# Optimization experiments

Hardware: AMD Instinct MI355X
Metric: run time of the kernel (lower is better)

The kernel has to match this reference:

```python
import jax, jax.numpy as jnp
import numpy as np

NUM_EXPERTS_TOTAL = 9  # 8 routed + 1 shared (shared expert is also routed via softmax in this module)
TOP_K = 2


def setup_inputs() -> dict:
    key = jax.random.key(0)
    k0, k1, k2, k3, k4 = jax.random.split(key, 5)
    B, S, H, I = 2, 2048, 1024, 2816
    E = NUM_EXPERTS_TOTAL
    x = jax.random.normal(k0, (B, S, H), dtype=jnp.float32)
    Wr = (jax.random.normal(k1, (H, E), dtype=jnp.float32) * 0.02)          # router (no bias)
    Wg = (jax.random.normal(k2, (E, H, I), dtype=jnp.float32) * 0.02)       # gate_proj per expert
    Wu = (jax.random.normal(k3, (E, H, I), dtype=jnp.float32) * 0.02)       # up_proj per expert
    Wd = (jax.random.normal(k4, (E, I, H), dtype=jnp.float32) * 0.02)       # down_proj per expert
    return {"x": x, "Wr": Wr, "Wg": Wg, "Wu": Wu, "Wd": Wd}


def reference(x, Wr, Wg, Wu, Wd):
    B, S, H = x.shape
    E = NUM_EXPERTS_TOTAL
    T = B * S

    # Router: softmax over all 9 experts, then top-2 and renormalize
    logits = jnp.einsum('bsh,he->bse', x, Wr)
    probs = jax.nn.softmax(logits, axis=-1)
    topk_w, topk_idx = jax.lax.top_k(probs, TOP_K)                 # [B,S,K]
    topk_w = topk_w / jnp.sum(topk_w, axis=-1, keepdims=True)

    xf = x.reshape(T, H)
    wf = topk_w.reshape(T, TOP_K)
    idxf = topk_idx.reshape(T, TOP_K)

    # Per-token combine weight for each expert (0 if not selected)
    cw = jnp.zeros((T, E), dtype=x.dtype).at[jnp.arange(T)[:, None], idxf].add(wf)  # [T,E]

    # SwiGLU MLP for every expert (tokens with cw==0 contribute nothing)
    gate = jax.nn.silu(jnp.einsum('th,ehi->tei', xf, Wg))          # [T,E,I]
    hidden = gate * jnp.einsum('th,ehi->tei', xf, Wu)              # [T,E,I]
    out = jnp.einsum('tei,eih,te->th', hidden, Wd, cw)             # weighted combine
    return out.reshape(B, S, H)
```

## Files before the change

### kernel.cpp

```cpp
#include <hip/hip_runtime.h>
#include <cstdint>
#include <cstddef>

#define T_TOK 4096
#define H_DIM 1024
#define I_DIM 2816
#define E_NUM 9
#define MAXTILE 76

typedef __bf16 bf16;
typedef bf16 bf16x4 __attribute__((ext_vector_type(4)));
typedef bf16 bf16x8 __attribute__((ext_vector_type(8)));
typedef float f32x4 __attribute__((ext_vector_type(4)));

constexpr int BM = 128, BN = 128, BK = 32;
constexpr int HTILE = BM * BK;
constexpr size_t HI = (size_t)H_DIM * I_DIM;

constexpr int XCAST_BLKS  = T_TOK * H_DIM / 2048;
constexpr int TGU_BLKS    = (I_DIM / 64) * (H_DIM / 64) * 2 * E_NUM;
constexpr int TD_BLKS     = (H_DIM / 64) * (I_DIM / 64) * E_NUM;
constexpr int ROUTER_BLKS = T_TOK / 4;
constexpr int PRE_BLKS    = XCAST_BLKS + TGU_BLKS + TD_BLKS + ROUTER_BLKS;

#define GL16(gp, lp)                                                                   \
  __builtin_amdgcn_global_load_lds((const __attribute__((address_space(1))) void*)(gp), \
                                   (__attribute__((address_space(3))) void*)(lp), 16, 0, 0)

__device__ __forceinline__ void transpose_tile(const float* __restrict__ src,
                                               bf16* __restrict__ dst, int R, int C,
                                               int bx, int by) {
  __shared__ float tile[64 * 64];
  int r0 = by * 64, c0 = bx * 64;
  int t = threadIdx.x;
#pragma unroll
  for (int h = 0; h < 4; ++h) {
    int idx = h * 256 + t;
    int row = idx >> 4;
    int col = (idx & 15) * 4;
    GL16(src + (size_t)(r0 + row) * C + c0 + col, &tile[idx * 4]);
  }
  __syncthreads();
  int oc = t >> 2;
  int q  = t & 3;
  bf16x8 w0, w1;
#pragma unroll
  for (int j = 0; j < 8; ++j) w0[j] = (bf16)tile[(q * 16 + j) * 64 + oc];
#pragma unroll
  for (int j = 0; j < 8; ++j) w1[j] = (bf16)tile[(q * 16 + 8 + j) * 64 + oc];
  bf16* dp = dst + (size_t)(c0 + oc) * R + r0 + q * 16;
  *reinterpret_cast<bf16x8*>(dp)     = w0;
  *reinterpret_cast<bf16x8*>(dp + 8) = w1;
}

__global__ __launch_bounds__(256) void k_prepass(const float* __restrict__ x,
                                                 bf16* __restrict__ xb,
                                                 const float* __restrict__ Wg,
                                                 const float* __restrict__ Wu,
                                                 const float* __restrict__ Wd,
                                                 bf16* __restrict__ WgT,
                                                 bf16* __restrict__ WuT,
                                                 bf16* __restrict__ WdT,
                                                 const float* __restrict__ Wr,
                                                 int* __restrict__ ridx,
                                                 float* __restrict__ rw,
                                                 int* __restrict__ counts) {
  int b = blockIdx.x;

  if (b < XCAST_BLKS) {
    size_t i = ((size_t)b * 256 + threadIdx.x) * 8;
    float4 a = *reinterpret_cast<const float4*>(x + i);
    float4 c = *reinterpret_cast<const float4*>(x + i + 4);
    bf16x8 v;
    v[0]=(bf16)a.x; v[1]=(bf16)a.y; v[2]=(bf16)a.z; v[3]=(bf16)a.w;
    v[4]=(bf16)c.x; v[5]=(bf16)c.y; v[6]=(bf16)c.z; v[7]=(bf16)c.w;
    *reinterpret_cast<bf16x8*>(xb + i) = v;
    return;
  }
  b -= XCAST_BLKS;

  if (b < TGU_BLKS) {
    int bx = b % (I_DIM / 64);
    int rest = b / (I_DIM / 64);
    int by = rest % (H_DIM / 64);
    int z  = rest / (H_DIM / 64);
    const float* src = (z < 9) ? (Wg + (size_t)z * HI) : (Wu + (size_t)(z - 9) * HI);
    bf16* dst = (z < 9) ? (WgT + (size_t)z * HI) : (WuT + (size_t)(z - 9) * HI);
    transpose_tile(src, dst, H_DIM, I_DIM, bx, by);
    return;
  }
  b -= TGU_BLKS;

  if (b < TD_BLKS) {
    int bx = b % (H_DIM / 64);
    int rest = b / (H_DIM / 64);
    int by = rest % (I_DIM / 64);
    int z  = rest / (I_DIM / 64);
    transpose_tile(Wd + (size_t)z * HI, WdT + (size_t)z * HI, I_DIM, H_DIM, bx, by);
    return;
  }
  b -= TD_BLKS;

  {
    int lane = threadIdx.x & 63;
    int wid  = threadIdx.x >> 6;
    int t = b * 4 + wid;
    const float* xr = x + (size_t)t * H_DIM;
    float acc[E_NUM];
#pragma unroll
    for (int e = 0; e < E_NUM; ++e) acc[e] = 0.f;
    for (int h = lane; h < H_DIM; h += 64) {
      float xv = xr[h];
      const float* wr = Wr + h * E_NUM;
#pragma unroll
      for (int e = 0; e < E_NUM; ++e) acc[e] += xv * wr[e];
    }
#pragma unroll
    for (int off = 32; off > 0; off >>= 1) {
#pragma unroll
      for (int e = 0; e < E_NUM; ++e) acc[e] += __shfl_xor(acc[e], off);
    }
    if (lane == 0) {
      int i0 = 0;
#pragma unroll
      for (int e = 1; e < E_NUM; ++e) if (acc[e] > acc[i0]) i0 = e;
      int i1 = (i0 == 0) ? 1 : 0;
#pragma unroll
      for (int e = 0; e < E_NUM; ++e) if (e != i0 && acc[e] > acc[i1]) i1 = e;
      float r  = expf(acc[i1] - acc[i0]);
      float w0 = 1.f / (1.f + r);
      float w1 = r / (1.f + r);
      ridx[2 * t]     = i0;
      ridx[2 * t + 1] = i1;
      rw[2 * t]     = w0;
      rw[2 * t + 1] = w1;
      atomicAdd(&counts[i0], 1);
      atomicAdd(&counts[i1], 1);
    }
  }
}

__global__ void k_scan(const int* __restrict__ counts, int* __restrict__ offsets,
                       int* __restrict__ cursor, int* __restrict__ tiles,
                       int* __restrict__ n_tiles) {
  if (threadIdx.x == 0) {
    int s = 0, nt = 0;
    for (int e = 0; e < E_NUM; ++e) {
      offsets[e] = s;
      int c = counts[e];
      for (int pt = 0; pt * BM < c && nt < MAXTILE; ++pt) tiles[nt++] = (e << 16) | pt;
      s += c;
    }
    offsets[E_NUM] = s;
    *n_tiles = nt;
  }
  if (threadIdx.x < E_NUM) cursor[threadIdx.x] = 0;
}

__global__ __launch_bounds__(256) void k_scatter(const int* __restrict__ ridx,
                                                 const int* __restrict__ offsets,
                                                 int* __restrict__ cursor,
                                                 int* __restrict__ perm) {
  int t = blockIdx.x * 256 + threadIdx.x;
  if (t >= T_TOK) return;
#pragma unroll
  for (int k = 0; k < 2; ++k) {
    int e = ridx[2 * t + k];
    int pos = atomicAdd(&cursor[e], 1);
    perm[offsets[e] + pos] = 2 * t + k;
  }
}

__global__ __launch_bounds__(256, 2) void k_gateup(const bf16* __restrict__ xb,
                                                   const bf16* __restrict__ WgT,
                                                   const bf16* __restrict__ WuT,
                                                   const int* __restrict__ perm,
                                                   const int* __restrict__ offsets,
                                                   const int* __restrict__ tiles,
                                                   const int* __restrict__ n_tiles,
                                                   bf16* __restrict__ hidden) {
  if ((int)blockIdx.y >= *n_tiles) return;
  int tv = tiles[blockIdx.y];
  int e = tv >> 16, pt = tv & 0xffff;
  int seg0 = offsets[e], cnt = offsets[e + 1] - seg0;
  int n0 = blockIdx.x * BN;

  __shared__ bf16 As[2 * HTILE];
  __shared__ bf16 Bg[2 * HTILE];
  __shared__ bf16 Bu[2 * HTILE];

  int tid = threadIdx.x, lane = tid & 63, wid = tid >> 6;
  int wm = wid >> 1, wn = wid & 1, l15 = lane & 15, l16 = lane >> 4;

  int srow1 = tid >> 2, srow2 = 64 + srow1;
  int kc = (tid & 3) * 8;
  int p1 = pt * BM + srow1, p2 = pt * BM + srow2;
  const bf16* a1 = xb + (size_t)(perm[seg0 + (p1 < cnt ? p1 : 0)] >> 1) * H_DIM + kc;
  const bf16* a2 = xb + (size_t)(perm[seg0 + (p2 < cnt ? p2 : 0)] >> 1) * H_DIM + kc;
  const bf16* g1 = WgT + ((size_t)e * I_DIM + n0 + srow1) * H_DIM + kc;
  const bf16* g2 = WgT + ((size_t)e * I_DIM + n0 + srow2) * H_DIM + kc;
  const bf16* u1 = WuT + ((size_t)e * I_DIM + n0 + srow1) * H_DIM + kc;
  const bf16* u2 = WuT + ((size_t)e * I_DIM + n0 + srow2) * H_DIM + kc;
  bf16* lA1 = &As[tid * 8];       bf16* lA2 = &As[2048 + tid * 8];
  bf16* lG1 = &Bg[tid * 8];       bf16* lG2 = &Bg[2048 + tid * 8];
  bf16* lU1 = &Bu[tid * 8];       bf16* lU2 = &Bu[2048 + tid * 8];

  f32x4 accg[4][4], accu[4][4];
#pragma unroll
  for (int m = 0; m < 4; ++m)
#pragma unroll
    for (int n = 0; n < 4; ++n) {
      accg[m][n] = (f32x4){0.f, 0.f, 0.f, 0.f};
      accu[m][n] = (f32x4){0.f, 0.f, 0.f, 0.f};
    }

  for (int k0 = 0; k0 < H_DIM; k0 += 2 * BK) {
    GL16(a1 + k0, lA1);            GL16(a2 + k0, lA2);
    GL16(a1 + k0 + BK, lA1 + HTILE); GL16(a2 + k0 + BK, lA2 + HTILE);
    GL16(g1 + k0, lG1);            GL16(g2 + k0, lG2);
    GL16(g1 + k0 + BK, lG1 + HTILE); GL16(g2 + k0 + BK, lG2 + HTILE);
    GL16(u1 + k0, lU1);            GL16(u2 + k0, lU2);
    GL16(u1 + k0 + BK, lU1 + HTILE); GL16(u2 + k0 + BK, lU2 + HTILE);
    __syncthreads();

#pragma unroll
    for (int kk = 0; kk < 2; ++kk) {
      const bf16* Ab = &As[kk * HTILE];
      const bf16* Gb = &Bg[kk * HTILE];
      const bf16* Ub = &Bu[kk * HTILE];
      bf16x8 af[4], bg[4], bu[4];
#pragma unroll
      for (int m = 0; m < 4; ++m)
        af[m] = *reinterpret_cast<const bf16x8*>(&Ab[(wm * 64 + m * 16 + l15) * BK + l16 * 8]);
#pragma unroll
      for (int n = 0; n < 4; ++n) {
        bg[n] = *reinterpret_cast<const bf16x8*>(&Gb[(wn * 64 + n * 16 + l15) * BK + l16 * 8]);
        bu[n] = *reinterpret_cast<const bf16x8*>(&Ub[(wn * 64 + n * 16 + l15) * BK + l16 * 8]);
      }
#pragma unroll
      for (int m = 0; m < 4; ++m)
#pragma unroll
        for (int n = 0; n < 4; ++n) {
          accg[m][n] = __builtin_amdgcn_mfma_f32_16x16x32_bf16(af[m], bg[n], accg[m][n], 0, 0, 0);
          accu[m][n] = __builtin_amdgcn_mfma_f32_16x16x32_bf16(af[m], bu[n], accu[m][n], 0, 0, 0);
        }
    }
    __syncthreads();
  }

#pragma unroll
  for (int m = 0; m < 4; ++m) {
#pragma unroll
    for (int r = 0; r < 4; ++r) {
      int p_glob = pt * BM + wm * 64 + m * 16 + l16 * 4 + r;
      if (p_glob < cnt) {
        bf16* hrow = hidden + (size_t)(seg0 + p_glob) * I_DIM;
#pragma unroll
        for (int n = 0; n < 4; ++n) {
          int col = n0 + wn * 64 + n * 16 + l15;
          float g = accg[m][n][r];
          float u = accu[m][n][r];
          float h = g / (1.f + __expf(-g)) * u;
          hrow[col] = (bf16)h;
        }
      }
    }
  }
}

__global__ __launch_bounds__(256, 2) void k_down(const bf16* __restrict__ hidden,
                                                 const bf16* __restrict__ WdT,
                                                 const int* __restrict__ perm,
                                                 const int* __restrict__ offsets,
                                                 const int* __restrict__ tiles,
                                                 const int* __restrict__ n_tiles,
                                                 bf16* __restrict__ pair_half) {
  if ((int)blockIdx.y >= *n_tiles) return;
  int tv = tiles[blockIdx.y];
  int e = tv >> 16, pt = tv & 0xffff;
  int seg0 = offsets[e], cnt = offsets[e + 1] - seg0;
  int n0 = blockIdx.x * BN;
  int kz = blockIdx.z * (I_DIM / 2);
  bf16* pout = pair_half + (size_t)blockIdx.z * 2 * T_TOK * H_DIM;

  __shared__ bf16 As[2 * HTILE];
  __shared__ bf16 Bs[2 * HTILE];

  int tid = threadIdx.x, lane = tid & 63, wid = tid >> 6;
  int wm = wid >> 1, wn = wid & 1, l15 = lane & 15, l16 = lane >> 4;

  int srow1 = tid >> 2, srow2 = 64 + srow1;
  int kc = (tid & 3) * 8;
  int p1 = pt * BM + srow1, p2 = pt * BM + srow2;
  const bf16* a1 = hidden + (size_t)(seg0 + (p1 < cnt ? p1 : 0)) * I_DIM + kz + kc;
  const bf16* a2 = hidden + (size_t)(seg0 + (p2 < cnt ? p2 : 0)) * I_DIM + kz + kc;
  const bf16* b1 = WdT + ((size_t)e * H_DIM + n0 + srow1) * I_DIM + kz + kc;
  const bf16* b2 = WdT + ((size_t)e * H_DIM + n0 + srow2) * I_DIM + kz + kc;
  bf16* lA1 = &As[tid * 8];  bf16* lA2 = &As[2048 + tid * 8];
  bf16* lB1 = &Bs[tid * 8];  bf16* lB2 = &Bs[2048 + tid * 8];

  f32x4 acc[4][4];
#pragma unroll
  for (int m = 0; m < 4; ++m)
#pragma unroll
    for (int n = 0; n < 4; ++n) acc[m][n] = (f32x4){0.f, 0.f, 0.f, 0.f};

  for (int k0 = 0; k0 < I_DIM / 2; k0 += 2 * BK) {
    GL16(a1 + k0, lA1);            GL16(a2 + k0, lA2);
    GL16(a1 + k0 + BK, lA1 + HTILE); GL16(a2 + k0 + BK, lA2 + HTILE);
    GL16(b1 + k0, lB1);            GL16(b2 + k0, lB2);
    GL16(b1 + k0 + BK, lB1 + HTILE); GL16(b2 + k0 + BK, lB2 + HTILE);
    __syncthreads();

#pragma unroll
    for (int kk = 0; kk < 2; ++kk) {
      const bf16* Ab = &As[kk * HTILE];
      const bf16* Bb = &Bs[kk * HTILE];
      bf16x8 af[4], bfr[4];
#pragma unroll
      for (int m = 0; m < 4; ++m)
        af[m] = *reinterpret_cast<const bf16x8*>(&Ab[(wm * 64 + m * 16 + l15) * BK + l16 * 8]);
#pragma unroll
      for (int n = 0; n < 4; ++n)
        bfr[n] = *reinterpret_cast<const bf16x8*>(&Bb[(wn * 64 + n * 16 + l15) * BK + l16 * 8]);
#pragma unroll
      for (int m = 0; m < 4; ++m)
#pragma unroll
        for (int n = 0; n < 4; ++n)
          acc[m][n] = __builtin_amdgcn_mfma_f32_16x16x32_bf16(af[m], bfr[n], acc[m][n], 0, 0, 0);
    }
    __syncthreads();
  }

#pragma unroll
  for (int m = 0; m < 4; ++m) {
#pragma unroll
    for (int r = 0; r < 4; ++r) {
      int p_glob = pt * BM + wm * 64 + m * 16 + l16 * 4 + r;
      if (p_glob < cnt) {
        int pair = perm[seg0 + p_glob];
        bf16* orow = pout + (size_t)pair * H_DIM;
#pragma unroll
        for (int n = 0; n < 4; ++n) {
          int col = n0 + wn * 64 + n * 16 + l15;
          orow[col] = (bf16)acc[m][n][r];
        }
      }
    }
  }
}

__global__ __launch_bounds__(256) void k_combine(const bf16* __restrict__ pair_half,
                                                 const float* __restrict__ rw,
                                                 float* __restrict__ out) {
  int t = blockIdx.x;
  int c = threadIdx.x;
  const bf16* z0 = pair_half;
  const bf16* z1 = pair_half + (size_t)2 * T_TOK * H_DIM;
  float w0 = rw[2 * t];
  float w1 = rw[2 * t + 1];
  size_t r0 = (size_t)(2 * t) * H_DIM + c * 4;
  size_t r1 = (size_t)(2 * t + 1) * H_DIM + c * 4;
  bf16x4 a0 = *reinterpret_cast<const bf16x4*>(z0 + r0);
  bf16x4 a1 = *reinterpret_cast<const bf16x4*>(z1 + r0);
  bf16x4 b0 = *reinterpret_cast<const bf16x4*>(z0 + r1);
  bf16x4 b1 = *reinterpret_cast<const bf16x4*>(z1 + r1);
  float4 o;
  o.x = w0 * ((float)a0[0] + (float)a1[0]) + w1 * ((float)b0[0] + (float)b1[0]);
  o.y = w0 * ((float)a0[1] + (float)a1[1]) + w1 * ((float)b0[1] + (float)b1[1]);
  o.z = w0 * ((float)a0[2] + (float)a1[2]) + w1 * ((float)b0[2] + (float)b1[2]);
  o.w = w0 * ((float)a0[3] + (float)a1[3]) + w1 * ((float)b0[3] + (float)b1[3]);
  *reinterpret_cast<float4*>(out + (size_t)t * H_DIM + c * 4) = o;
}

extern "C" void kernel_launch(void* const* d_in, const int* in_sizes, int n_in,
                              void* d_out, int out_size, void* d_ws, size_t ws_size,
                              hipStream_t stream) {
  const float* x  = (const float*)d_in[0];
  const float* Wr = (const float*)d_in[1];
  const float* Wg = (const float*)d_in[2];
  const float* Wu = (const float*)d_in[3];
  const float* Wd = (const float*)d_in[4];
  float* out = (float*)d_out;

  char* ws = (char*)d_ws;
  int*   counts  = (int*)(ws);
  int*   cursor  = (int*)(ws + 256);
  int*   offsets = (int*)(ws + 512);
  int*   n_tiles = (int*)(ws + 768);
  int*   tiles   = (int*)(ws + 1024);
  int*   ridx    = (int*)(ws + 64 * 1024);
  float* rw      = (float*)(ws + 128 * 1024);
  int*   perm    = (int*)(ws + 192 * 1024);
  bf16*  xb      = (bf16*)(ws + (1ull << 20));
  bf16*  WgT     = (bf16*)(ws + (16ull << 20));
  bf16*  WuT     = (bf16*)(ws + (66ull << 20));
  bf16*  WdT     = (bf16*)(ws + (116ull << 20));
  bf16*  hidden  = (bf16*)(ws + (166ull << 20));
  bf16*  pair_half = (bf16*)(ws + (212ull << 20));

  hipMemsetAsync(counts, 0, 64, stream);
  k_prepass<<<dim3(PRE_BLKS), dim3(256), 0, stream>>>(
      x, xb, Wg, Wu, Wd, WgT, WuT, WdT, Wr, ridx, rw, counts);
  k_scan<<<dim3(1), dim3(64), 0, stream>>>(counts, offsets, cursor, tiles, n_tiles);
  k_scatter<<<dim3((T_TOK + 255) / 256), dim3(256), 0, stream>>>(ridx, offsets, cursor, perm);
  k_gateup<<<dim3(I_DIM / BN, MAXTILE), dim3(256), 0, stream>>>(
      xb, WgT, WuT, perm, offsets, tiles, n_tiles, hidden);
  k_down<<<dim3(H_DIM / BN, MAXTILE, 2), dim3(256), 0, stream>>>(
      hidden, WdT, perm, offsets, tiles, n_tiles, pair_half);
  k_combine<<<dim3(T_TOK), dim3(256), 0, stream>>>(pair_half, rw, out);
}
```

Measured before the change: 454.5 us.

## Move down-proj weight transpose into gate/up kernel to overlap with GEMM

The Wd transpose-and-cast blocks are moved out of the prepass kernel and appended as extra blocks of the gate/up GEMM launch. The launch becomes a flat 1D grid whose leading blocks run the gate/up GEMM and whose trailing blocks transpose Wd, and the two roles share one shared-memory buffer. The goal is to shorten the critical path: the prepass no longer waits on the Wd transpose, and that memory-bound work can fill idle compute units, including slots left by GEMM tiles that exit early. The cost is that the transpose blocks now compete with the GEMM for bandwidth and CU slots, and they run at the GEMM kernel's larger shared-memory footprint and occupancy limits.

After: 441.4 us. 2.9% less time.

```diff
diff --git a/kernel.cpp b/kernel.cpp
--- a/kernel.cpp
+++ b/kernel.cpp
@@ -19,18 +19,21 @@
 
 constexpr int XCAST_BLKS  = T_TOK * H_DIM / 2048;
 constexpr int TGU_BLKS    = (I_DIM / 64) * (H_DIM / 64) * 2 * E_NUM;
-constexpr int TD_BLKS     = (H_DIM / 64) * (I_DIM / 64) * E_NUM;
 constexpr int ROUTER_BLKS = T_TOK / 4;
-constexpr int PRE_BLKS    = XCAST_BLKS + TGU_BLKS + TD_BLKS + ROUTER_BLKS;
+constexpr int PRE1_BLKS   = XCAST_BLKS + TGU_BLKS + ROUTER_BLKS;
+
+constexpr int GU_BLKS = (I_DIM / BN) * MAXTILE;
+constexpr int TD_BLKS = (H_DIM / 64) * (I_DIM / 64) * E_NUM;
+constexpr int MAIN1_BLKS = GU_BLKS + TD_BLKS;
 
 #define GL16(gp, lp)                                                                   \
   __builtin_amdgcn_global_load_lds((const __attribute__((address_space(1))) void*)(gp), \
                                    (__attribute__((address_space(3))) void*)(lp), 16, 0, 0)
 
-__device__ __forceinline__ void transpose_tile(const float* __restrict__ src,
+__device__ __forceinline__ void transpose_tile(float* __restrict__ tile,
+                                               const float* __restrict__ src,
                                                bf16* __restrict__ dst, int R, int C,
                                                int bx, int by) {
-  __shared__ float tile[64 * 64];
   int r0 = by * 64, c0 = bx * 64;
   int t = threadIdx.x;
 #pragma unroll
@@ -53,18 +56,17 @@
   *reinterpret_cast<bf16x8*>(dp + 8) = w1;
 }
 
-__global__ __launch_bounds__(256) void k_prepass(const float* __restrict__ x,
-                                                 bf16* __restrict__ xb,
-                                                 const float* __restrict__ Wg,
-                                                 const float* __restrict__ Wu,
-                                                 const float* __restrict__ Wd,
-                                                 bf16* __restrict__ WgT,
-                                                 bf16* __restrict__ WuT,
-                                                 bf16* __restrict__ WdT,
-                                                 const float* __restrict__ Wr,
-                                                 int* __restrict__ ridx,
-                                                 float* __restrict__ rw,
-                                                 int* __restrict__ counts) {
+__global__ __launch_bounds__(256) void k_pre1(const float* __restrict__ x,
+                                              bf16* __restrict__ xb,
+                                              const float* __restrict__ Wg,
+                                              const float* __restrict__ Wu,
+                                              bf16* __restrict__ WgT,
+                                              bf16* __restrict__ WuT,
+                                              const float* __restrict__ Wr,
+                                              int* __restrict__ ridx,
+                                              float* __restrict__ rw,
+                                              int* __restrict__ counts) {
+  __shared__ float tile[64 * 64];
   int b = blockIdx.x;
 
   if (b < XCAST_BLKS) {
@@ -86,20 +88,10 @@
     int z  = rest / (H_DIM / 64);
     const float* src = (z < 9) ? (Wg + (size_t)z * HI) : (Wu + (size_t)(z - 9) * HI);
     bf16* dst = (z < 9) ? (WgT + (size_t)z * HI) : (WuT + (size_t)(z - 9) * HI);
-    transpose_tile(src, dst, H_DIM, I_DIM, bx, by);
+    transpose_tile(tile, src, dst, H_DIM, I_DIM, bx, by);
     return;
   }
   b -= TGU_BLKS;
-
-  if (b < TD_BLKS) {
-    int bx = b % (H_DIM / 64);
-    int rest = b / (H_DIM / 64);
-    int by = rest % (I_DIM / 64);
-    int z  = rest / (I_DIM / 64);
-    transpose_tile(Wd + (size_t)z * HI, WdT + (size_t)z * HI, I_DIM, H_DIM, bx, by);
-    return;
-  }
-  b -= TD_BLKS;
 
   {
     int lane = threadIdx.x & 63;
@@ -171,23 +163,40 @@
   }
 }
 
-__global__ __launch_bounds__(256, 2) void k_gateup(const bf16* __restrict__ xb,
-                                                   const bf16* __restrict__ WgT,
-                                                   const bf16* __restrict__ WuT,
-                                                   const int* __restrict__ perm,
-                                                   const int* __restrict__ offsets,
-                                                   const int* __restrict__ tiles,
-                                                   const int* __restrict__ n_tiles,
-                                                   bf16* __restrict__ hidden) {
-  if ((int)blockIdx.y >= *n_tiles) return;
-  int tv = tiles[blockIdx.y];
+__global__ __launch_bounds__(256, 2) void k_main1(const bf16* __restrict__ xb,
+                                                  const bf16* __restrict__ WgT,
+                                                  const bf16* __restrict__ WuT,
+                                                  const int* __restrict__ perm,
+                                                  const int* __restrict__ offsets,
+                                                  const int* __restrict__ tiles,
+                                                  const int* __restrict__ n_tiles,
+                                                  bf16* __restrict__ hidden,
+                                                  const float* __restrict__ Wd,
+                                                  bf16* __restrict__ WdT) {
+  __shared__ char smem[6 * HTILE * 2];
+  int b = blockIdx.x;
+
+  if (b >= GU_BLKS) {
+    b -= GU_BLKS;
+    int bx = b % (H_DIM / 64);
+    int rest = b / (H_DIM / 64);
+    int by = rest % (I_DIM / 64);
+    int z  = rest / (I_DIM / 64);
+    transpose_tile((float*)smem, Wd + (size_t)z * HI, WdT + (size_t)z * HI,
+                   I_DIM, H_DIM, bx, by);
+    return;
+  }
+
+  int ty = b / (I_DIM / BN);
+  int n0 = (b % (I_DIM / BN)) * BN;
+  if (ty >= *n_tiles) return;
+  int tv = tiles[ty];
   int e = tv >> 16, pt = tv & 0xffff;
   int seg0 = offsets[e], cnt = offsets[e + 1] - seg0;
-  int n0 = blockIdx.x * BN;
-
-  __shared__ bf16 As[2 * HTILE];
-  __shared__ bf16 Bg[2 * HTILE];
-  __shared__ bf16 Bu[2 * HTILE];
+
+  bf16* As = (bf16*)smem;
+  bf16* Bg = As + 2 * HTILE;
+  bf16* Bu = As + 4 * HTILE;
 
   int tid = threadIdx.x, lane = tid & 63, wid = tid >> 6;
   int wm = wid >> 1, wn = wid & 1, l15 = lane & 15, l16 = lane >> 4;
@@ -400,12 +409,12 @@
   bf16*  pair_half = (bf16*)(ws + (212ull << 20));
 
   hipMemsetAsync(counts, 0, 64, stream);
-  k_prepass<<<dim3(PRE_BLKS), dim3(256), 0, stream>>>(
-      x, xb, Wg, Wu, Wd, WgT, WuT, WdT, Wr, ridx, rw, counts);
+  k_pre1<<<dim3(PRE1_BLKS), dim3(256), 0, stream>>>(
+      x, xb, Wg, Wu, WgT, WuT, Wr, ridx, rw, counts);
   k_scan<<<dim3(1), dim3(64), 0, stream>>>(counts, offsets, cursor, tiles, n_tiles);
   k_scatter<<<dim3((T_TOK + 255) / 256), dim3(256), 0, stream>>>(ridx, offsets, cursor, perm);
-  k_gateup<<<dim3(I_DIM / BN, MAXTILE), dim3(256), 0, stream>>>(
-      xb, WgT, WuT, perm, offsets, tiles, n_tiles, hidden);
+  k_main1<<<dim3(MAIN1_BLKS), dim3(256), 0, stream>>>(
+      xb, WgT, WuT, perm, offsets, tiles, n_tiles, hidden, Wd, WdT);
   k_down<<<dim3(H_DIM / BN, MAXTILE, 2), dim3(256), 0, stream>>>(
       hidden, WdT, perm, offsets, tiles, n_tiles, pair_half);
   k_combine<<<dim3(T_TOK), dim3(256), 0, stream>>>(pair_half, rw, out);
```
